# Optimization experiments

Hardware: AMD Instinct MI355X
Metric: run time of the kernel (lower is better)

## Reference

```python
import jax, jax.numpy as jnp
import numpy as np

EPS = 1e-7
TAU = 2.0  # curr_temp = max_temp at init
GROUPS = 2
NUM_CODES = 320


def setup_inputs() -> dict:
    key = jax.random.key(0)
    k1, k2, k3, k4 = jax.random.split(key, 4)
    B, T, C = 8, 2048, 1024
    GV = GROUPS * NUM_CODES  # 640
    D = 256
    x = jax.random.normal(k1, (B, T, C), dtype=jnp.float32)
    W = jax.random.normal(k2, (GV, C), dtype=jnp.float32)  # nn.init.normal_(std=1)
    b = jnp.zeros((GV,), dtype=jnp.float32)
    codebook = jax.random.uniform(k3, (1, GV, D), dtype=jnp.float32)  # uniform_ init
    u = jax.random.uniform(k4, (B * T * GROUPS, NUM_CODES), dtype=jnp.float32,
                           minval=1e-10, maxval=1.0)
    gumbel_noise = -jnp.log(-jnp.log(u))
    return {"x": x, "W": W, "b": b, "codebook": codebook, "gumbel_noise": gumbel_noise}


def reference(x, W, b, codebook, gumbel_noise):
    B, T, C = x.shape
    N = B * T
    G, V = GROUPS, NUM_CODES
    D = codebook.shape[-1]

    # weight projection -> logits [N, G*V]
    logits = jnp.einsum('nc,vc->nv', x.reshape(N, C), W) + b
    l = logits.reshape(N * G, V)

    # hard codes (no-grad path in torch)
    k = jnp.argmax(l, axis=-1)
    hard_x = jax.nn.one_hot(k, V, dtype=l.dtype).reshape(N, G, V)
    hard_probs = jax.lax.stop_gradient(hard_x).mean(axis=0)  # [G, V]
    code_perplexity = jnp.exp(-jnp.sum(hard_probs * jnp.log(hard_probs + EPS), axis=-1)).sum()

    avg_probs = jax.nn.softmax(l.reshape(N, G, V), axis=-1).mean(axis=0)  # [G, V]
    prob_perplexity = jnp.exp(-jnp.sum(avg_probs * jnp.log(avg_probs + EPS), axis=-1)).sum()

    # gumbel-softmax, hard=True with straight-through (training path)
    y_soft = jax.nn.softmax((l + gumbel_noise) / TAU, axis=-1)  # [N*G, V]
    idx = jnp.argmax(y_soft, axis=-1)
    y_hard = jax.nn.one_hot(idx, V, dtype=y_soft.dtype)
    y = y_hard + y_soft - jax.lax.stop_gradient(y_soft)

    # combine with codebook: (onehot-ish weights) @ codebook per group
    q = jnp.einsum('ngv,gvd->ngd', y.reshape(N, G, V), codebook.reshape(G, V, D))
    q = q.reshape(B, T, G * D)

    num_vars = G * V
    diversity_loss = (num_vars - prob_perplexity) / num_vars
    return q, code_perplexity, prob_perplexity, diversity_loss
```

## Files before the change

### kernel.cpp

```cpp
#include <hip/hip_runtime.h>

#define N_ROWS 16384
#define C_DIM  1024
#define GV     640
#define V_DIM  320
#define G_DIM  2
#define D_DIM  256
#define MROWS  64
#define FBLKS  (N_ROWS / MROWS)
#define NBUCKET 64

typedef __attribute__((ext_vector_type(8))) _Float16 half8;
typedef __attribute__((ext_vector_type(4))) _Float16 half4v;
typedef __attribute__((ext_vector_type(4))) float float4v;

#define LDS_AS(p) ((__attribute__((address_space(3))) unsigned int*)(p))
#define GLB_AS(p) ((const __attribute__((address_space(1))) unsigned int*)(p))

__global__ __launch_bounds__(256) void wsplit_kernel(const float* __restrict__ src,
                                                     _Float16* __restrict__ dst,
                                                     int* __restrict__ zr) {
  const int t = blockIdx.x * 256 + threadIdx.x;
  zr[t] = 0;
  const int n = t % GV;
  const int cc = t / GV;
  const int k = cc * 8;
  const float4 v0 = *(const float4*)(src + (size_t)n * C_DIM + k);
  const float4 v1 = *(const float4*)(src + (size_t)n * C_DIM + k + 4);
  half8 h;
  h[0] = (_Float16)v0.x; h[1] = (_Float16)v0.y; h[2] = (_Float16)v0.z; h[3] = (_Float16)v0.w;
  h[4] = (_Float16)v1.x; h[5] = (_Float16)v1.y; h[6] = (_Float16)v1.z; h[7] = (_Float16)v1.w;
  *(half8*)(dst + (size_t)t * 8) = h;
}

__global__ __launch_bounds__(512, 2) void fused_kernel(
    const float* __restrict__ x,
    const _Float16* __restrict__ whT,
    const float* __restrict__ bias,
    const float* __restrict__ gn,
    const float* __restrict__ cb,
    float* __restrict__ q,
    float* __restrict__ mf,
    int* __restrict__ mi) {
  __shared__ __align__(16) char smemU[98304];
  _Float16* BhL = (_Float16*)smemU;
  _Float16* AhL = (_Float16*)(smemU + 81920);
  _Float16* AlL = (_Float16*)(smemU + 90112);
  float* Ldump  = (float*)smemU;
  __shared__ float accL[GV];
  __shared__ int   cntL[GV];

  const int tid = threadIdx.x;
  const int lane = tid & 63;
  const int w = tid >> 6;
  const int m0 = blockIdx.x * MROWS;
  const int frow = lane & 15;
  const int quad = lane >> 4;

  for (int e = tid; e < GV; e += 512) { accL[e] = 0.0f; cntL[e] = 0; }

  const int ar = tid >> 3;
  const int ak = (tid & 7) * 4;
  const int ac = ak >> 3;
  const int ah_off = ak & 7;
  const float* xp = x + (size_t)(m0 + ar) * C_DIM + ak;

  float4v acc[4][5];
#pragma unroll
  for (int i = 0; i < 4; ++i)
#pragma unroll
    for (int j = 0; j < 5; ++j) acc[i][j] = (float4v)0.0f;

  auto stageB = [&](int kb, _Float16* Bh) {
    const _Float16* bsrc = whT + (size_t)kb * 2560 * 8;
#pragma unroll
    for (int s = 0; s < 5; ++s) {
      const int c = s * 512 + tid;
      __builtin_amdgcn_global_load_lds(GLB_AS(bsrc + (size_t)c * 8),
                                       LDS_AS(Bh + c * 8), 16, 0, 0);
    }
  };
  auto splitA = [&](const float4& a4, _Float16* Ah, _Float16* Al) {
    const _Float16 h0 = (_Float16)a4.x, h1 = (_Float16)a4.y;
    const _Float16 h2 = (_Float16)a4.z, h3 = (_Float16)a4.w;
    half4v hv, lv;
    hv[0] = h0; hv[1] = h1; hv[2] = h2; hv[3] = h3;
    lv[0] = (_Float16)(a4.x - (float)h0);
    lv[1] = (_Float16)(a4.y - (float)h1);
    lv[2] = (_Float16)(a4.z - (float)h2);
    lv[3] = (_Float16)(a4.w - (float)h3);
    *(half4v*)&Ah[(ac * 64 + ar) * 8 + ah_off] = hv;
    *(half4v*)&Al[(ac * 64 + ar) * 8 + ah_off] = lv;
  };

  float4 a4 = *(const float4*)xp;
  stageB(0, BhL);
  splitA(a4, AhL, AlL);
  a4 = *(const float4*)(xp + 32);
  __syncthreads();

  for (int kb = 0; kb < 32; ++kb) {
    const int cur = kb & 1;
    _Float16* BhC = BhL + cur * 20480;
    _Float16* AhC = AhL + cur * 2048;
    _Float16* AlC = AlL + cur * 2048;

    if (kb < 31) {
      const int nxt = cur ^ 1;
      stageB(kb + 1, BhL + nxt * 20480);
      splitA(a4, AhL + nxt * 2048, AlL + nxt * 2048);
      if (kb < 30) a4 = *(const float4*)(xp + (kb + 2) * 32);
    }

    half8 ah[4], al[4];
#pragma unroll
    for (int i = 0; i < 4; ++i) {
      ah[i] = *(const half8*)&AhC[(quad * 64 + 16 * i + frow) * 8];
      al[i] = *(const half8*)&AlC[(quad * 64 + 16 * i + frow) * 8];
    }
#pragma unroll
    for (int j = 0; j < 5; ++j) {
      const half8 bh = *(const half8*)&BhC[(quad * 640 + 80 * w + 16 * j + frow) * 8];
#pragma unroll
      for (int i = 0; i < 4; ++i) {
        acc[i][j] = __builtin_amdgcn_mfma_f32_16x16x32_f16(ah[i], bh, acc[i][j], 0, 0, 0);
        acc[i][j] = __builtin_amdgcn_mfma_f32_16x16x32_f16(al[i], bh, acc[i][j], 0, 0, 0);
      }
    }
    __syncthreads();
  }

  float bw[5];
#pragma unroll
  for (int j = 0; j < 5; ++j) bw[j] = bias[80 * w + 16 * j + frow];

#pragma unroll
  for (int g = 0; g < G_DIM; ++g) {
    __syncthreads();
    if ((w >> 2) == g) {
      const int cg0 = 80 * (w & 3) + frow;
#pragma unroll
      for (int i = 0; i < 4; ++i)
#pragma unroll
        for (int j = 0; j < 5; ++j)
#pragma unroll
          for (int r = 0; r < 4; ++r)
            Ldump[(16 * i + 4 * quad + r) * 321 + cg0 + 16 * j] = acc[i][j][r] + bw[j];
    }
    __syncthreads();

    float pacc5[5] = {0.0f, 0.0f, 0.0f, 0.0f, 0.0f};
#pragma unroll
    for (int rr = 0; rr < 8; ++rr) {
      const int row = w * 8 + rr;
      const int n = m0 + row;
      const float* gp = gn + (size_t)(2 * n + g) * V_DIM;

      float l[5], t[5];
#pragma unroll
      for (int j = 0; j < 5; ++j) {
        l[j] = Ldump[row * 321 + lane + 64 * j];
        t[j] = (l[j] + gp[lane + 64 * j]) * 0.5f;
      }

      float m = l[0]; int mi_ = lane;
#pragma unroll
      for (int j = 1; j < 5; ++j) {
        const int v = lane + 64 * j;
        if (l[j] > m) { m = l[j]; mi_ = v; }
      }
#pragma unroll
      for (int off = 32; off > 0; off >>= 1) {
        const float om = __shfl_xor(m, off, 64);
        const int omi = __shfl_xor(mi_, off, 64);
        if (om > m || (om == m && omi < mi_)) { m = om; mi_ = omi; }
      }
      if (lane == 0) atomicAdd(&cntL[g * V_DIM + mi_], 1);

      float e[5], s = 0.0f;
#pragma unroll
      for (int j = 0; j < 5; ++j) { e[j] = expf(l[j] - m); s += e[j]; }
#pragma unroll
      for (int off = 32; off > 0; off >>= 1) s += __shfl_xor(s, off, 64);
      const float inv = 1.0f / s;
#pragma unroll
      for (int j = 0; j < 5; ++j) pacc5[j] += e[j] * inv;

      float tm = t[0]; int ti = lane;
#pragma unroll
      for (int j = 1; j < 5; ++j) {
        const int v = lane + 64 * j;
        if (t[j] > tm) { tm = t[j]; ti = v; }
      }
#pragma unroll
      for (int off = 32; off > 0; off >>= 1) {
        const float om = __shfl_xor(tm, off, 64);
        const int omi = __shfl_xor(ti, off, 64);
        if (om > tm || (om == tm && omi < ti)) { tm = om; ti = omi; }
      }
      float ts = 0.0f;
#pragma unroll
      for (int j = 0; j < 5; ++j) ts += expf(t[j] - tm);
#pragma unroll
      for (int off = 32; off > 0; off >>= 1) ts += __shfl_xor(ts, off, 64);
      const float sv = 1.0f / ts;
      const float yv = (1.0f + sv) - sv;

      const float4 c4 = ((const float4*)(cb + ((size_t)(g * V_DIM + ti)) * D_DIM))[lane];
      float4 o4;
      o4.x = yv * c4.x; o4.y = yv * c4.y; o4.z = yv * c4.z; o4.w = yv * c4.w;
      ((float4*)q)[(size_t)n * 128 + g * 64 + lane] = o4;
    }
#pragma unroll
    for (int j = 0; j < 5; ++j)
      atomicAdd(&accL[g * V_DIM + lane + 64 * j], pacc5[j]);
  }

  __syncthreads();
  const size_t pb = (size_t)(blockIdx.x & (NBUCKET - 1)) * GV;
  for (int e = tid; e < GV; e += 512) {
    atomicAdd(&mf[pb + e], accL[e]);
    atomicAdd(&mi[pb + e], cntL[e]);
  }
}

__global__ __launch_bounds__(640) void finalize_kernel(
    const float* __restrict__ mf, const int* __restrict__ mi,
    float* __restrict__ out3) {
  __shared__ float sA[G_DIM];
  __shared__ float sC[G_DIM];
  const int t = threadIdx.x;
  if (t < G_DIM) { sA[t] = 0.0f; sC[t] = 0.0f; }
  __syncthreads();

  const int g = t / V_DIM;
  float f = 0.0f;
  int   c = 0;
#pragma unroll 8
  for (int b = 0; b < NBUCKET; ++b) {
    f += mf[(size_t)b * GV + t];
    c += mi[(size_t)b * GV + t];
  }
  const float pa = f * (1.0f / 16384.0f);
  const float ph = (float)c * (1.0f / 16384.0f);
  float a = pa * logf(pa + 1e-7f);
  float h = ph * logf(ph + 1e-7f);
#pragma unroll
  for (int off = 32; off > 0; off >>= 1) {
    a += __shfl_xor(a, off, 64);
    h += __shfl_xor(h, off, 64);
  }
  if ((t & 63) == 0) {
    atomicAdd(&sA[g], a);
    atomicAdd(&sC[g], h);
  }
  __syncthreads();
  if (t == 0) {
    const float code_p = expf(-sC[0]) + expf(-sC[1]);
    const float prob_p = expf(-sA[0]) + expf(-sA[1]);
    out3[0] = code_p;
    out3[1] = prob_p;
    out3[2] = ((float)GV - prob_p) / (float)GV;
  }
}

extern "C" void kernel_launch(void* const* d_in, const int* in_sizes, int n_in,
                              void* d_out, int out_size, void* d_ws, size_t ws_size,
                              hipStream_t stream) {
  const float* x  = (const float*)d_in[0];
  const float* W  = (const float*)d_in[1];
  const float* b  = (const float*)d_in[2];
  const float* cb = (const float*)d_in[3];
  const float* gn = (const float*)d_in[4];
  float* out = (float*)d_out;

  char* ws = (char*)d_ws;
  _Float16* whT = (_Float16*)ws;
  float* mf = (float*)(ws + 1310720);
  int*   mi = (int*)  (ws + 1474560);

  wsplit_kernel<<<(GV * C_DIM / 8) / 256, 256, 0, stream>>>(W, whT, (int*)mf);

  fused_kernel<<<FBLKS, 512, 0, stream>>>(x, whT, b, gn, cb, out, mf, mi);

  finalize_kernel<<<1, 640, 0, stream>>>(mf, mi, out + (size_t)N_ROWS * 512);
}
```

Baseline: 210.7 us.

## Split fused GEMM+softmax into separate GEMM and epilogue kernels via workspace logits

The GEMM writes the biased logits to a global workspace buffer, and a separate high-occupancy epilogue kernel then does the argmax, softmax statistics, Gumbel selection and codebook gather, one wave per row-group. The aim is to stop the serial epilogue, which uses only 8 waves per 64-row block, from stalling the MFMA-bound GEMM, and to give the memory-bound gather phase more parallelism. The cost is a round trip of about 42 MB of logits through HBM, an extra launch, and more LDS atomics per row. The old fused path is kept as a fallback when the workspace is too small.

```diff
diff --git a/kernel.cpp b/kernel.cpp
--- a/kernel.cpp
+++ b/kernel.cpp
@@ -33,22 +33,15 @@
   *(half8*)(dst + (size_t)t * 8) = h;
 }
 
-__global__ __launch_bounds__(512, 2) void fused_kernel(
+__global__ __launch_bounds__(512, 2) void gemm_kernel(
     const float* __restrict__ x,
     const _Float16* __restrict__ whT,
     const float* __restrict__ bias,
-    const float* __restrict__ gn,
-    const float* __restrict__ cb,
-    float* __restrict__ q,
-    float* __restrict__ mf,
-    int* __restrict__ mi) {
+    float* __restrict__ logits) {
   __shared__ __align__(16) char smemU[98304];
   _Float16* BhL = (_Float16*)smemU;
   _Float16* AhL = (_Float16*)(smemU + 81920);
   _Float16* AlL = (_Float16*)(smemU + 90112);
-  float* Ldump  = (float*)smemU;
-  __shared__ float accL[GV];
-  __shared__ int   cntL[GV];
 
   const int tid = threadIdx.x;
   const int lane = tid & 63;
@@ -56,8 +49,6 @@
   const int m0 = blockIdx.x * MROWS;
   const int frow = lane & 15;
   const int quad = lane >> 4;
-
-  for (int e = tid; e < GV; e += 512) { accL[e] = 0.0f; cntL[e] = 0; }
 
   const int ar = tid >> 3;
   const int ak = (tid & 7) * 4;
@@ -134,6 +125,201 @@
 #pragma unroll
   for (int j = 0; j < 5; ++j) bw[j] = bias[80 * w + 16 * j + frow];
 
+  float* lp = logits + (size_t)(m0 + 4 * quad) * GV + 80 * w + frow;
+#pragma unroll
+  for (int i = 0; i < 4; ++i)
+#pragma unroll
+    for (int j = 0; j < 5; ++j)
+#pragma unroll
+      for (int r = 0; r < 4; ++r)
+        lp[(size_t)(16 * i + r) * GV + 16 * j] = acc[i][j][r] + bw[j];
+}
+
+__global__ __launch_bounds__(256, 8) void epilogue_kernel(
+    const float* __restrict__ logits,
+    const float* __restrict__ gn,
+    const float* __restrict__ cb,
+    float* __restrict__ q,
+    float* __restrict__ mf,
+    int* __restrict__ mi) {
+  __shared__ float accL[GV];
+  __shared__ int   cntL[GV];
+  const int tid = threadIdx.x;
+  const int lane = tid & 63;
+  const int w = tid >> 6;
+
+  for (int e = tid; e < GV; e += 256) { accL[e] = 0.0f; cntL[e] = 0; }
+  __syncthreads();
+
+#pragma unroll 1
+  for (int tt = 0; tt < 4; ++tt) {
+    const int task = blockIdx.x * 16 + w * 4 + tt;
+    const int n = task >> 1;
+    const int g = task & 1;
+
+    const float* lrow = logits + (size_t)n * GV + g * V_DIM;
+    const float* gp = gn + (size_t)(2 * n + g) * V_DIM;
+
+    float l[5], t[5];
+#pragma unroll
+    for (int j = 0; j < 5; ++j) {
+      l[j] = lrow[lane + 64 * j];
+      t[j] = (l[j] + gp[lane + 64 * j]) * 0.5f;
+    }
+
+    float m = l[0]; int mi_ = lane;
+#pragma unroll
+    for (int j = 1; j < 5; ++j) {
+      const int v = lane + 64 * j;
+      if (l[j] > m) { m = l[j]; mi_ = v; }
+    }
+#pragma unroll
+    for (int off = 32; off > 0; off >>= 1) {
+      const float om = __shfl_xor(m, off, 64);
+      const int omi = __shfl_xor(mi_, off, 64);
+      if (om > m || (om == m && omi < mi_)) { m = om; mi_ = omi; }
+    }
+    if (lane == 0) atomicAdd(&cntL[g * V_DIM + mi_], 1);
+
+    float e[5], s = 0.0f;
+#pragma unroll
+    for (int j = 0; j < 5; ++j) { e[j] = expf(l[j] - m); s += e[j]; }
+#pragma unroll
+    for (int off = 32; off > 0; off >>= 1) s += __shfl_xor(s, off, 64);
+    const float inv = 1.0f / s;
+#pragma unroll
+    for (int j = 0; j < 5; ++j)
+      atomicAdd(&accL[g * V_DIM + lane + 64 * j], e[j] * inv);
+
+    float tm = t[0]; int ti = lane;
+#pragma unroll
+    for (int j = 1; j < 5; ++j) {
+      const int v = lane + 64 * j;
+      if (t[j] > tm) { tm = t[j]; ti = v; }
+    }
+#pragma unroll
+    for (int off = 32; off > 0; off >>= 1) {
+      const float om = __shfl_xor(tm, off, 64);
+      const int omi = __shfl_xor(ti, off, 64);
+      if (om > tm || (om == tm && omi < ti)) { tm = om; ti = omi; }
+    }
+    float ts = 0.0f;
+#pragma unroll
+    for (int j = 0; j < 5; ++j) ts += expf(t[j] - tm);
+#pragma unroll
+    for (int off = 32; off > 0; off >>= 1) ts += __shfl_xor(ts, off, 64);
+    const float sv = 1.0f / ts;
+    const float yv = (1.0f + sv) - sv;
+
+    const float4 c4 = ((const float4*)(cb + ((size_t)(g * V_DIM + ti)) * D_DIM))[lane];
+    float4 o4;
+    o4.x = yv * c4.x; o4.y = yv * c4.y; o4.z = yv * c4.z; o4.w = yv * c4.w;
+    ((float4*)q)[(size_t)n * 128 + g * 64 + lane] = o4;
+  }
+
+  __syncthreads();
+  const size_t pb = (size_t)(blockIdx.x & (NBUCKET - 1)) * GV;
+  for (int e = tid; e < GV; e += 256) {
+    atomicAdd(&mf[pb + e], accL[e]);
+    atomicAdd(&mi[pb + e], cntL[e]);
+  }
+}
+
+__global__ __launch_bounds__(512, 2) void fused_kernel(
+    const float* __restrict__ x, const _Float16* __restrict__ whT,
+    const float* __restrict__ bias, const float* __restrict__ gn,
+    const float* __restrict__ cb, float* __restrict__ q,
+    float* __restrict__ mf, int* __restrict__ mi) {
+  __shared__ __align__(16) char smemU[98304];
+  _Float16* BhL = (_Float16*)smemU;
+  _Float16* AhL = (_Float16*)(smemU + 81920);
+  _Float16* AlL = (_Float16*)(smemU + 90112);
+  float* Ldump  = (float*)smemU;
+  __shared__ float accL[GV];
+  __shared__ int   cntL[GV];
+
+  const int tid = threadIdx.x;
+  const int lane = tid & 63;
+  const int w = tid >> 6;
+  const int m0 = blockIdx.x * MROWS;
+  const int frow = lane & 15;
+  const int quad = lane >> 4;
+
+  for (int e = tid; e < GV; e += 512) { accL[e] = 0.0f; cntL[e] = 0; }
+
+  const int ar = tid >> 3;
+  const int ak = (tid & 7) * 4;
+  const int ac = ak >> 3;
+  const int ah_off = ak & 7;
+  const float* xp = x + (size_t)(m0 + ar) * C_DIM + ak;
+
+  float4v acc[4][5];
+#pragma unroll
+  for (int i = 0; i < 4; ++i)
+#pragma unroll
+    for (int j = 0; j < 5; ++j) acc[i][j] = (float4v)0.0f;
+
+  auto stageB = [&](int kb, _Float16* Bh) {
+    const _Float16* bsrc = whT + (size_t)kb * 2560 * 8;
+#pragma unroll
+    for (int s = 0; s < 5; ++s) {
+      const int c = s * 512 + tid;
+      __builtin_amdgcn_global_load_lds(GLB_AS(bsrc + (size_t)c * 8),
+                                       LDS_AS(Bh + c * 8), 16, 0, 0);
+    }
+  };
+  auto splitA = [&](const float4& a4, _Float16* Ah, _Float16* Al) {
+    const _Float16 h0 = (_Float16)a4.x, h1 = (_Float16)a4.y;
+    const _Float16 h2 = (_Float16)a4.z, h3 = (_Float16)a4.w;
+    half4v hv, lv;
+    hv[0] = h0; hv[1] = h1; hv[2] = h2; hv[3] = h3;
+    lv[0] = (_Float16)(a4.x - (float)h0);
+    lv[1] = (_Float16)(a4.y - (float)h1);
+    lv[2] = (_Float16)(a4.z - (float)h2);
+    lv[3] = (_Float16)(a4.w - (float)h3);
+    *(half4v*)&Ah[(ac * 64 + ar) * 8 + ah_off] = hv;
+    *(half4v*)&Al[(ac * 64 + ar) * 8 + ah_off] = lv;
+  };
+
+  float4 a4 = *(const float4*)xp;
+  stageB(0, BhL);
+  splitA(a4, AhL, AlL);
+  a4 = *(const float4*)(xp + 32);
+  __syncthreads();
+
+  for (int kb = 0; kb < 32; ++kb) {
+    const int cur = kb & 1;
+    _Float16* BhC = BhL + cur * 20480;
+    _Float16* AhC = AhL + cur * 2048;
+    _Float16* AlC = AlL + cur * 2048;
+    if (kb < 31) {
+      const int nxt = cur ^ 1;
+      stageB(kb + 1, BhL + nxt * 20480);
+      splitA(a4, AhL + nxt * 2048, AlL + nxt * 2048);
+      if (kb < 30) a4 = *(const float4*)(xp + (kb + 2) * 32);
+    }
+    half8 ah[4], al[4];
+#pragma unroll
+    for (int i = 0; i < 4; ++i) {
+      ah[i] = *(const half8*)&AhC[(quad * 64 + 16 * i + frow) * 8];
+      al[i] = *(const half8*)&AlC[(quad * 64 + 16 * i + frow) * 8];
+    }
+#pragma unroll
+    for (int j = 0; j < 5; ++j) {
+      const half8 bh = *(const half8*)&BhC[(quad * 640 + 80 * w + 16 * j + frow) * 8];
+#pragma unroll
+      for (int i = 0; i < 4; ++i) {
+        acc[i][j] = __builtin_amdgcn_mfma_f32_16x16x32_f16(ah[i], bh, acc[i][j], 0, 0, 0);
+        acc[i][j] = __builtin_amdgcn_mfma_f32_16x16x32_f16(al[i], bh, acc[i][j], 0, 0, 0);
+      }
+    }
+    __syncthreads();
+  }
+
+  float bw[5];
+#pragma unroll
+  for (int j = 0; j < 5; ++j) bw[j] = bias[80 * w + 16 * j + frow];
+
 #pragma unroll
   for (int g = 0; g < G_DIM; ++g) {
     __syncthreads();
@@ -155,14 +341,12 @@
       const int row = w * 8 + rr;
       const int n = m0 + row;
       const float* gp = gn + (size_t)(2 * n + g) * V_DIM;
-
       float l[5], t[5];
 #pragma unroll
       for (int j = 0; j < 5; ++j) {
         l[j] = Ldump[row * 321 + lane + 64 * j];
         t[j] = (l[j] + gp[lane + 64 * j]) * 0.5f;
       }
-
       float m = l[0]; int mi_ = lane;
 #pragma unroll
       for (int j = 1; j < 5; ++j) {
@@ -176,7 +360,6 @@
         if (om > m || (om == m && omi < mi_)) { m = om; mi_ = omi; }
       }
       if (lane == 0) atomicAdd(&cntL[g * V_DIM + mi_], 1);
-
       float e[5], s = 0.0f;
 #pragma unroll
       for (int j = 0; j < 5; ++j) { e[j] = expf(l[j] - m); s += e[j]; }
@@ -185,7 +368,6 @@
       const float inv = 1.0f / s;
 #pragma unroll
       for (int j = 0; j < 5; ++j) pacc5[j] += e[j] * inv;
-
       float tm = t[0]; int ti = lane;
 #pragma unroll
       for (int j = 1; j < 5; ++j) {
@@ -205,7 +387,6 @@
       for (int off = 32; off > 0; off >>= 1) ts += __shfl_xor(ts, off, 64);
       const float sv = 1.0f / ts;
       const float yv = (1.0f + sv) - sv;
-
       const float4 c4 = ((const float4*)(cb + ((size_t)(g * V_DIM + ti)) * D_DIM))[lane];
       float4 o4;
       o4.x = yv * c4.x; o4.y = yv * c4.y; o4.z = yv * c4.z; o4.w = yv * c4.w;
@@ -278,10 +459,18 @@
   _Float16* whT = (_Float16*)ws;
   float* mf = (float*)(ws + 1310720);
   int*   mi = (int*)  (ws + 1474560);
+  float* logits = (float*)(ws + 1638400);
+
+  const size_t needed = 1638400 + (size_t)N_ROWS * GV * 4;
 
   wsplit_kernel<<<(GV * C_DIM / 8) / 256, 256, 0, stream>>>(W, whT, (int*)mf);
 
-  fused_kernel<<<FBLKS, 512, 0, stream>>>(x, whT, b, gn, cb, out, mf, mi);
+  if (ws_size >= needed) {
+    gemm_kernel<<<FBLKS, 512, 0, stream>>>(x, whT, b, logits);
+    epilogue_kernel<<<(N_ROWS * G_DIM) / 16, 256, 0, stream>>>(logits, gn, cb, out, mf, mi);
+  } else {
+    fused_kernel<<<FBLKS, 512, 0, stream>>>(x, whT, b, gn, cb, out, mf, mi);
+  }
 
   finalize_kernel<<<1, 640, 0, stream>>>(mf, mi, out + (size_t)N_ROWS * 512);
 }
```

New measurement: 253.1 us. 1.2x slower.

## Remap softmax epilogue to 16 threads per row with vectorized loads

Applied to the files above, without the earlier changes.

The post-GEMM epilogue now gives each row to 16 threads, each holding 20 contiguous logits read as float4, instead of one wavefront per row with 5 strided values per lane. Rows are handled in two halves of 32 so the LDS dump buffer is smaller. This cuts shuffle-reduction depth from 6 to 4 steps, runs the two argmax and two sum reductions together, and vectorizes the gumbel noise loads. In exchange, the per-row probability accumulation becomes many LDS atomics per thread rather than one register accumulation per wave, and there are extra barriers.

```diff
diff --git a/kernel.cpp b/kernel.cpp
--- a/kernel.cpp
+++ b/kernel.cpp
@@ -134,86 +134,97 @@
 #pragma unroll
   for (int j = 0; j < 5; ++j) bw[j] = bias[80 * w + 16 * j + frow];
 
-#pragma unroll
+  const int rl = tid >> 4;
+  const int h  = tid & 15;
+
+#pragma unroll 1
   for (int g = 0; g < G_DIM; ++g) {
-    __syncthreads();
-    if ((w >> 2) == g) {
-      const int cg0 = 80 * (w & 3) + frow;
-#pragma unroll
-      for (int i = 0; i < 4; ++i)
-#pragma unroll
-        for (int j = 0; j < 5; ++j)
-#pragma unroll
-          for (int r = 0; r < 4; ++r)
-            Ldump[(16 * i + 4 * quad + r) * 321 + cg0 + 16 * j] = acc[i][j][r] + bw[j];
-    }
-    __syncthreads();
-
-    float pacc5[5] = {0.0f, 0.0f, 0.0f, 0.0f, 0.0f};
-#pragma unroll
-    for (int rr = 0; rr < 8; ++rr) {
-      const int row = w * 8 + rr;
-      const int n = m0 + row;
-      const float* gp = gn + (size_t)(2 * n + g) * V_DIM;
-
-      float l[5], t[5];
-#pragma unroll
-      for (int j = 0; j < 5; ++j) {
-        l[j] = Ldump[row * 321 + lane + 64 * j];
-        t[j] = (l[j] + gp[lane + 64 * j]) * 0.5f;
-      }
-
-      float m = l[0]; int mi_ = lane;
-#pragma unroll
-      for (int j = 1; j < 5; ++j) {
-        const int v = lane + 64 * j;
-        if (l[j] > m) { m = l[j]; mi_ = v; }
-      }
-#pragma unroll
-      for (int off = 32; off > 0; off >>= 1) {
+#pragma unroll 1
+    for (int hh = 0; hh < 2; ++hh) {
+      __syncthreads();
+      if ((w >> 2) == g) {
+        const int cg0 = 80 * (w & 3) + frow;
+#pragma unroll
+        for (int ii = 0; ii < 2; ++ii) {
+          const int i = 2 * hh + ii;
+#pragma unroll
+          for (int j = 0; j < 5; ++j)
+#pragma unroll
+            for (int r = 0; r < 4; ++r)
+              Ldump[(16 * ii + 4 * quad + r) * 324 + cg0 + 16 * j] = acc[i][j][r] + bw[j];
+        }
+      }
+      __syncthreads();
+
+      const int n = m0 + hh * 32 + rl;
+      const float* gp = gn + (size_t)(2 * n + g) * V_DIM + 20 * h;
+      const float* lp = Ldump + rl * 324 + 20 * h;
+
+      float4v L[5], T[5];
+      float m = -3.0e38f, tm = -3.0e38f;
+      int midx = 0, tidx = 0;
+#pragma unroll
+      for (int cc = 0; cc < 5; ++cc) {
+        const float4v lv = *(const float4v*)(lp + 4 * cc);
+        const float4v gv = *(const float4v*)(gp + 4 * cc);
+        float4v tv;
+#pragma unroll
+        for (int e2 = 0; e2 < 4; ++e2) tv[e2] = (lv[e2] + gv[e2]) * 0.5f;
+        L[cc] = lv; T[cc] = tv;
+#pragma unroll
+        for (int e2 = 0; e2 < 4; ++e2) {
+          const int v = 20 * h + 4 * cc + e2;
+          if (lv[e2] > m)  { m = lv[e2];  midx = v; }
+          if (tv[e2] > tm) { tm = tv[e2]; tidx = v; }
+        }
+      }
+#pragma unroll
+      for (int off = 8; off > 0; off >>= 1) {
         const float om = __shfl_xor(m, off, 64);
-        const int omi = __shfl_xor(mi_, off, 64);
-        if (om > m || (om == m && omi < mi_)) { m = om; mi_ = omi; }
-      }
-      if (lane == 0) atomicAdd(&cntL[g * V_DIM + mi_], 1);
-
-      float e[5], s = 0.0f;
-#pragma unroll
-      for (int j = 0; j < 5; ++j) { e[j] = expf(l[j] - m); s += e[j]; }
-#pragma unroll
-      for (int off = 32; off > 0; off >>= 1) s += __shfl_xor(s, off, 64);
-      const float inv = 1.0f / s;
-#pragma unroll
-      for (int j = 0; j < 5; ++j) pacc5[j] += e[j] * inv;
-
-      float tm = t[0]; int ti = lane;
-#pragma unroll
-      for (int j = 1; j < 5; ++j) {
-        const int v = lane + 64 * j;
-        if (t[j] > tm) { tm = t[j]; ti = v; }
-      }
-#pragma unroll
-      for (int off = 32; off > 0; off >>= 1) {
-        const float om = __shfl_xor(tm, off, 64);
-        const int omi = __shfl_xor(ti, off, 64);
-        if (om > tm || (om == tm && omi < ti)) { tm = om; ti = omi; }
-      }
-      float ts = 0.0f;
-#pragma unroll
-      for (int j = 0; j < 5; ++j) ts += expf(t[j] - tm);
-#pragma unroll
-      for (int off = 32; off > 0; off >>= 1) ts += __shfl_xor(ts, off, 64);
-      const float sv = 1.0f / ts;
+        const int   oi = __shfl_xor(midx, off, 64);
+        if (om > m || (om == m && oi < midx)) { m = om; midx = oi; }
+        const float ot  = __shfl_xor(tm, off, 64);
+        const int   oti = __shfl_xor(tidx, off, 64);
+        if (ot > tm || (ot == tm && oti < tidx)) { tm = ot; tidx = oti; }
+      }
+
+      float sl = 0.0f, st = 0.0f;
+#pragma unroll
+      for (int cc = 0; cc < 5; ++cc)
+#pragma unroll
+        for (int e2 = 0; e2 < 4; ++e2) {
+          const float el = expf(L[cc][e2] - m);
+          L[cc][e2] = el;
+          sl += el;
+          st += expf(T[cc][e2] - tm);
+        }
+#pragma unroll
+      for (int off = 8; off > 0; off >>= 1) {
+        sl += __shfl_xor(sl, off, 64);
+        st += __shfl_xor(st, off, 64);
+      }
+      const float inv = 1.0f / sl;
+      const float sv = 1.0f / st;
       const float yv = (1.0f + sv) - sv;
 
-      const float4 c4 = ((const float4*)(cb + ((size_t)(g * V_DIM + ti)) * D_DIM))[lane];
-      float4 o4;
-      o4.x = yv * c4.x; o4.y = yv * c4.y; o4.z = yv * c4.z; o4.w = yv * c4.w;
-      ((float4*)q)[(size_t)n * 128 + g * 64 + lane] = o4;
-    }
-#pragma unroll
-    for (int j = 0; j < 5; ++j)
-      atomicAdd(&accL[g * V_DIM + lane + 64 * j], pacc5[j]);
+#pragma unroll
+      for (int cc = 0; cc < 5; ++cc)
+#pragma unroll
+        for (int e2 = 0; e2 < 4; ++e2)
+          atomicAdd(&accL[g * V_DIM + 20 * h + 4 * cc + e2], L[cc][e2] * inv);
+      if (h == 0) atomicAdd(&cntL[g * V_DIM + midx], 1);
+
+      const float4v* cbp = (const float4v*)cb + (size_t)(g * V_DIM + tidx) * 64;
+      float4v* qp = (float4v*)q + (size_t)n * 128 + g * 64;
+#pragma unroll
+      for (int k2 = 0; k2 < 4; ++k2) {
+        const float4v c4 = cbp[h + 16 * k2];
+        float4v o4;
+#pragma unroll
+        for (int e2 = 0; e2 < 4; ++e2) o4[e2] = yv * c4[e2];
+        qp[h + 16 * k2] = o4;
+      }
+    }
   }
 
   __syncthreads();
```

Result: slower. 459.9 us (+118.3%).
